# Kernel optimization log

Hardware: AMD Instinct MI355X
Metric: run time of the kernel (lower is better)

The kernel has to match this reference:

```python
import jax, jax.numpy as jnp
import numpy as np

ALPHA = 0.25
GAMMA = 2.0
W_CLASS = 2.0
W_BBOX = 5.0
W_GIOU = 2.0
EPS_LOG = 1e-8
EPS_DIV = 1e-6


def box_cxcywh_to_xyxy(b):
    cx, cy, w, h = b[..., 0], b[..., 1], b[..., 2], b[..., 3]
    return jnp.stack([cx - 0.5 * w, cy - 0.5 * h, cx + 0.5 * w, cy + 0.5 * h], axis=-1)


def generalized_box_iou(b1, b2):
    # b1: [N,4], b2: [M,4], xyxy -> giou [N,M]
    area1 = (b1[:, 2] - b1[:, 0]) * (b1[:, 3] - b1[:, 1])
    area2 = (b2[:, 2] - b2[:, 0]) * (b2[:, 3] - b2[:, 1])
    lt = jnp.maximum(b1[:, None, :2], b2[None, :, :2])
    rb = jnp.minimum(b1[:, None, 2:], b2[None, :, 2:])
    wh = jnp.maximum(rb - lt, 0.0)
    inter = wh[..., 0] * wh[..., 1]
    union = area1[:, None] + area2[None, :] - inter
    iou = inter / jnp.maximum(union, EPS_DIV)
    lt_e = jnp.minimum(b1[:, None, :2], b2[None, :, :2])
    rb_e = jnp.maximum(b1[:, None, 2:], b2[None, :, 2:])
    wh_e = jnp.maximum(rb_e - lt_e, 0.0)
    enclosing = wh_e[..., 0] * wh_e[..., 1]
    return iou - (enclosing - union) / jnp.maximum(enclosing, EPS_DIV)


def setup_inputs() -> dict:
    key = jax.random.key(0)
    k1, k2, k3, k4 = jax.random.split(key, 4)
    B, Q, C, T = 16, 900, 91, 4800  # T = 16 images * 300 targets
    pred_logits = jax.random.normal(k1, (B, Q, C), dtype=jnp.float32)
    pred_boxes = jax.random.uniform(k2, (B, Q, 4), dtype=jnp.float32)  # cxcywh in [0,1]
    tgt_ids = jax.random.randint(k3, (T,), 1, C + 1)  # 1-based labels (code uses tgt_ids - 1)
    tgt_boxes = jax.random.uniform(k4, (T, 4), dtype=jnp.float32)
    return {"pred_logits": pred_logits, "pred_boxes": pred_boxes,
            "tgt_ids": tgt_ids, "tgt_boxes": tgt_boxes}


def reference(pred_logits, pred_boxes, tgt_ids, tgt_boxes):
    B, Q, C = pred_logits.shape
    pl = jax.nn.sigmoid(pred_logits.reshape(B * Q, C))   # [BQ, C]
    pb = pred_boxes.reshape(B * Q, 4)                    # [BQ, 4]

    # focal-style class cost
    neg_cost = (1.0 - ALPHA) * pl ** GAMMA * (-jnp.log(1.0 - pl + EPS_LOG))
    pos_cost = ALPHA * (1.0 - pl) ** GAMMA * (-jnp.log(pl + EPS_LOG))
    cost_class = (pos_cost - neg_cost)[:, tgt_ids - 1]   # [BQ, T]

    # L1 box cost (cdist, p=1)
    cost_bbox = jnp.sum(jnp.abs(pb[:, None, :] - tgt_boxes[None, :, :]), axis=-1)  # [BQ, T]

    # negative generalized IoU cost
    cost_giou = -generalized_box_iou(box_cxcywh_to_xyxy(pb), box_cxcywh_to_xyxy(tgt_boxes))

    Cmat = W_CLASS * cost_class + W_BBOX * cost_bbox + W_GIOU * cost_giou
    return Cmat.reshape(B, Q, -1)  # [B, Q, T]
```

## Files before the change

### kernel.cpp

```cpp
#include <hip/hip_runtime.h>

typedef float f32x4 __attribute__((ext_vector_type(4)));

constexpr int kB = 16, kQ = 900, kC = 91, kT = 4800;
constexpr int kBQ = kB * kQ;
constexpr int kTI = 16;
constexpr int kJT = 4;
constexpr int kBT = 256;
constexpr int kJB = kBT * kJT;
constexpr int kCDS = 20;

__global__ __launch_bounds__(256)
void class_cost_kernel(const float* __restrict__ logits,
                       float* __restrict__ cd, int n) {
    int idx = blockIdx.x * 256 + threadIdx.x;
    if (idx >= n) return;
    float x = logits[idx];
    float p = 1.0f / (1.0f + expf(-x));
    float omp = 1.0f - p;
    float pos = 0.25f * omp * omp * (-logf(p + 1e-8f));
    float neg = 0.75f * p * p * (-logf(omp + 1e-8f));
    cd[idx] = 2.0f * (pos - neg) + 2.0f;
}

__global__ __launch_bounds__(256, 4)
void cost_kernel(const float* __restrict__ pred_boxes,
                 const int*   __restrict__ tgt_ids,
                 const float* __restrict__ tgt_boxes,
                 const float* __restrict__ cd,
                 float*       __restrict__ out) {
    __shared__ float lds_cdT[kC * kCDS];

    const int tid = threadIdx.x;
    const int i0  = blockIdx.y * kTI;
    const int j0  = blockIdx.x * kJB + tid * kJT;

    for (int k = tid; k < kTI * kC; k += kBT) {
        int i = k / kC, c = k - i * kC;
        lds_cdT[c * kCDS + i] = cd[(i0 + i) * kC + c];
    }
    __syncthreads();

    if (j0 + kJT > kT) return;

    int4 ids = *reinterpret_cast<const int4*>(&tgt_ids[j0]);
    const float* rowp[kJT] = {
        &lds_cdT[(ids.x - 1) * kCDS], &lds_cdT[(ids.y - 1) * kCDS],
        &lds_cdT[(ids.z - 1) * kCDS], &lds_cdT[(ids.w - 1) * kCDS] };

    float tcx[kJT], tcy[kJT], tw[kJT], th[kJT];
    float tx0[kJT], ty0[kJT], tx1[kJT], ty1[kJT], ta[kJT];
    #pragma unroll
    for (int q = 0; q < kJT; ++q) {
        float4 tb = reinterpret_cast<const float4*>(tgt_boxes)[j0 + q];
        tcx[q] = tb.x; tcy[q] = tb.y; tw[q] = tb.z; th[q] = tb.w;
        tx0[q] = tb.x - 0.5f * tb.z;  ty0[q] = tb.y - 0.5f * tb.w;
        tx1[q] = tb.x + 0.5f * tb.z;  ty1[q] = tb.y + 0.5f * tb.w;
        ta[q]  = tb.z * tb.w;
    }

    const size_t row0 = (size_t)i0 * kT + j0;

    #pragma unroll
    for (int ig = 0; ig < kTI / 4; ++ig) {
        f32x4 cdv[kJT];
        #pragma unroll
        for (int q = 0; q < kJT; ++q)
            cdv[q] = *reinterpret_cast<const f32x4*>(rowp[q] + ig * 4);

        #pragma unroll
        for (int i2 = 0; i2 < 4; ++i2) {
            const int ii = ig * 4 + i2;
            const float4 pb = reinterpret_cast<const float4*>(pred_boxes)[i0 + ii];
            const float pcx = pb.x, pcy = pb.y, pw = pb.z, ph = pb.w;
            const float px0 = pcx - 0.5f * pw, py0 = pcy - 0.5f * ph;
            const float px1 = pcx + 0.5f * pw, py1 = pcy + 0.5f * ph;
            const float pa  = pw * ph;

            f32x4 res;
            #pragma unroll
            for (int q = 0; q < kJT; ++q) {
                const float cdvq = cdv[q][i2];

                float dx = pcx - tcx[q], dy = pcy - tcy[q];
                float dw = pw  - tw[q],  dh = ph  - th[q];
                float l1 = (fabsf(dx) + fabsf(dy)) + (fabsf(dw) + fabsf(dh));

                float lx = fmaxf(px0, tx0[q]), ly = fmaxf(py0, ty0[q]);
                float rx = fminf(px1, tx1[q]), ry = fminf(py1, ty1[q]);
                float iwr = rx - lx, ihr = ry - ly;
                float inter = fmaxf(iwr, 0.f) * fmaxf(ihr, 0.f);

                float ew  = (pw + tw[q]) - iwr;
                float eh  = (ph + th[q]) - ihr;
                float enc = ew * eh;
                float uni = (pa + ta[q]) - inter;

                float rcpu = __builtin_amdgcn_rcpf(fmaxf(uni, 1e-6f));
                float rcpe = __builtin_amdgcn_rcpf(fmaxf(enc, 1e-6f));

                float c = fmaf(5.0f, l1, cdvq);
                c = fmaf(-2.0f, inter * rcpu, c);
                c = fmaf(-2.0f, uni * rcpe, c);
                res[q] = c;
            }

            *reinterpret_cast<f32x4*>(&out[row0 + (size_t)ii * kT]) = res;
        }
    }
}

extern "C" void kernel_launch(void* const* d_in, const int* in_sizes, int n_in,
                              void* d_out, int out_size, void* d_ws, size_t ws_size,
                              hipStream_t stream) {
    const float* logits  = (const float*)d_in[0];
    const float* pboxes  = (const float*)d_in[1];
    const int*   tids    = (const int*)d_in[2];
    const float* tboxes  = (const float*)d_in[3];
    float* out = (float*)d_out;
    float* cd  = (float*)d_ws;

    const int n_cd = kBQ * kC;
    class_cost_kernel<<<(n_cd + 255) / 256, 256, 0, stream>>>(logits, cd, n_cd);

    dim3 grid((kT + kJB - 1) / kJB, kBQ / kTI);
    cost_kernel<<<grid, 256, 0, stream>>>(pboxes, tids, tboxes, cd, out);
}
```

Baseline: 308.7 us.

## Fuse class-cost computation into the main cost kernel, loop over target tiles

Removes the separate sigmoid/focal class-cost kernel and its workspace round trip: each block now computes the class costs for its 8 query rows directly into LDS from the logits. Each block then loops over all target tiles instead of one tile per block, so the class-cost tile is computed once per row group rather than reloaded by every target-tile block. Row tile shrinks from 16 to 8 to keep the grid large. This drops a kernel launch and the intermediate array traffic, at the cost of less output work per LDS tile and a serial loop over five target tiles per block.

```diff
diff --git a/kernel.cpp b/kernel.cpp
--- a/kernel.cpp
+++ b/kernel.cpp
@@ -4,108 +4,103 @@
 
 constexpr int kB = 16, kQ = 900, kC = 91, kT = 4800;
 constexpr int kBQ = kB * kQ;
-constexpr int kTI = 16;
+constexpr int kTI = 8;
 constexpr int kJT = 4;
 constexpr int kBT = 256;
 constexpr int kJB = kBT * kJT;
-constexpr int kCDS = 20;
-
-__global__ __launch_bounds__(256)
-void class_cost_kernel(const float* __restrict__ logits,
-                       float* __restrict__ cd, int n) {
-    int idx = blockIdx.x * 256 + threadIdx.x;
-    if (idx >= n) return;
-    float x = logits[idx];
-    float p = 1.0f / (1.0f + expf(-x));
-    float omp = 1.0f - p;
-    float pos = 0.25f * omp * omp * (-logf(p + 1e-8f));
-    float neg = 0.75f * p * p * (-logf(omp + 1e-8f));
-    cd[idx] = 2.0f * (pos - neg) + 2.0f;
-}
+constexpr int kNT = (kT + kJB - 1) / kJB;
+constexpr int kCDS = 12;
 
 __global__ __launch_bounds__(256, 4)
-void cost_kernel(const float* __restrict__ pred_boxes,
-                 const int*   __restrict__ tgt_ids,
-                 const float* __restrict__ tgt_boxes,
-                 const float* __restrict__ cd,
-                 float*       __restrict__ out) {
+void fused_cost_kernel(const float* __restrict__ logits,
+                       const float* __restrict__ pred_boxes,
+                       const int*   __restrict__ tgt_ids,
+                       const float* __restrict__ tgt_boxes,
+                       float*       __restrict__ out) {
     __shared__ float lds_cdT[kC * kCDS];
 
     const int tid = threadIdx.x;
-    const int i0  = blockIdx.y * kTI;
-    const int j0  = blockIdx.x * kJB + tid * kJT;
+    const int i0  = blockIdx.x * kTI;
 
     for (int k = tid; k < kTI * kC; k += kBT) {
+        float x = logits[i0 * kC + k];
+        float p = 1.0f / (1.0f + expf(-x));
+        float omp = 1.0f - p;
+        float pos = 0.25f * omp * omp * (-logf(p + 1e-8f));
+        float neg = 0.75f * p * p * (-logf(omp + 1e-8f));
         int i = k / kC, c = k - i * kC;
-        lds_cdT[c * kCDS + i] = cd[(i0 + i) * kC + c];
+        lds_cdT[c * kCDS + i] = 2.0f * (pos - neg) + 2.0f;
     }
     __syncthreads();
 
-    if (j0 + kJT > kT) return;
+    for (int jt = 0; jt < kNT; ++jt) {
+        const int j0 = jt * kJB + tid * kJT;
+        if (j0 >= kT) continue;
 
-    int4 ids = *reinterpret_cast<const int4*>(&tgt_ids[j0]);
-    const float* rowp[kJT] = {
-        &lds_cdT[(ids.x - 1) * kCDS], &lds_cdT[(ids.y - 1) * kCDS],
-        &lds_cdT[(ids.z - 1) * kCDS], &lds_cdT[(ids.w - 1) * kCDS] };
+        int4 ids = *reinterpret_cast<const int4*>(&tgt_ids[j0]);
+        const float* rowp[kJT] = {
+            &lds_cdT[(ids.x - 1) * kCDS], &lds_cdT[(ids.y - 1) * kCDS],
+            &lds_cdT[(ids.z - 1) * kCDS], &lds_cdT[(ids.w - 1) * kCDS] };
 
-    float tcx[kJT], tcy[kJT], tw[kJT], th[kJT];
-    float tx0[kJT], ty0[kJT], tx1[kJT], ty1[kJT], ta[kJT];
-    #pragma unroll
-    for (int q = 0; q < kJT; ++q) {
-        float4 tb = reinterpret_cast<const float4*>(tgt_boxes)[j0 + q];
-        tcx[q] = tb.x; tcy[q] = tb.y; tw[q] = tb.z; th[q] = tb.w;
-        tx0[q] = tb.x - 0.5f * tb.z;  ty0[q] = tb.y - 0.5f * tb.w;
-        tx1[q] = tb.x + 0.5f * tb.z;  ty1[q] = tb.y + 0.5f * tb.w;
-        ta[q]  = tb.z * tb.w;
-    }
-
-    const size_t row0 = (size_t)i0 * kT + j0;
-
-    #pragma unroll
-    for (int ig = 0; ig < kTI / 4; ++ig) {
-        f32x4 cdv[kJT];
+        float tcx[kJT], tcy[kJT], tw[kJT], th[kJT];
+        float tx0[kJT], ty0[kJT], tx1[kJT], ty1[kJT], ta[kJT];
         #pragma unroll
-        for (int q = 0; q < kJT; ++q)
-            cdv[q] = *reinterpret_cast<const f32x4*>(rowp[q] + ig * 4);
+        for (int q = 0; q < kJT; ++q) {
+            float4 tb = reinterpret_cast<const float4*>(tgt_boxes)[j0 + q];
+            tcx[q] = tb.x; tcy[q] = tb.y; tw[q] = tb.z; th[q] = tb.w;
+            tx0[q] = tb.x - 0.5f * tb.z;  ty0[q] = tb.y - 0.5f * tb.w;
+            tx1[q] = tb.x + 0.5f * tb.z;  ty1[q] = tb.y + 0.5f * tb.w;
+            ta[q]  = tb.z * tb.w;
+        }
 
         #pragma unroll
-        for (int i2 = 0; i2 < 4; ++i2) {
-            const int ii = ig * 4 + i2;
-            const float4 pb = reinterpret_cast<const float4*>(pred_boxes)[i0 + ii];
-            const float pcx = pb.x, pcy = pb.y, pw = pb.z, ph = pb.w;
-            const float px0 = pcx - 0.5f * pw, py0 = pcy - 0.5f * ph;
-            const float px1 = pcx + 0.5f * pw, py1 = pcy + 0.5f * ph;
-            const float pa  = pw * ph;
+        for (int ig = 0; ig < kTI / 4; ++ig) {
+            f32x4 cdv[kJT];
+            #pragma unroll
+            for (int q = 0; q < kJT; ++q)
+                cdv[q] = *reinterpret_cast<const f32x4*>(rowp[q] + ig * 4);
 
-            f32x4 res;
             #pragma unroll
-            for (int q = 0; q < kJT; ++q) {
-                const float cdvq = cdv[q][i2];
+            for (int i2 = 0; i2 < 4; ++i2) {
+                const int ii = ig * 4 + i2;
+                const float4 pb =
+                    reinterpret_cast<const float4*>(pred_boxes)[i0 + ii];
+                const float pcx = pb.x, pcy = pb.y, pw = pb.z, ph = pb.w;
+                const float px0 = pcx - 0.5f * pw, py0 = pcy - 0.5f * ph;
+                const float px1 = pcx + 0.5f * pw, py1 = pcy + 0.5f * ph;
+                const float pa  = pw * ph;
 
-                float dx = pcx - tcx[q], dy = pcy - tcy[q];
-                float dw = pw  - tw[q],  dh = ph  - th[q];
-                float l1 = (fabsf(dx) + fabsf(dy)) + (fabsf(dw) + fabsf(dh));
+                f32x4 res;
+                #pragma unroll
+                for (int q = 0; q < kJT; ++q) {
+                    const float cdvq = cdv[q][i2];
 
-                float lx = fmaxf(px0, tx0[q]), ly = fmaxf(py0, ty0[q]);
-                float rx = fminf(px1, tx1[q]), ry = fminf(py1, ty1[q]);
-                float iwr = rx - lx, ihr = ry - ly;
-                float inter = fmaxf(iwr, 0.f) * fmaxf(ihr, 0.f);
+                    float dx = pcx - tcx[q], dy = pcy - tcy[q];
+                    float dw = pw  - tw[q],  dh = ph  - th[q];
+                    float l1 = (fabsf(dx) + fabsf(dy)) + (fabsf(dw) + fabsf(dh));
 
-                float ew  = (pw + tw[q]) - iwr;
-                float eh  = (ph + th[q]) - ihr;
-                float enc = ew * eh;
-                float uni = (pa + ta[q]) - inter;
+                    float lx = fmaxf(px0, tx0[q]), ly = fmaxf(py0, ty0[q]);
+                    float rx = fminf(px1, tx1[q]), ry = fminf(py1, ty1[q]);
+                    float iwr = rx - lx, ihr = ry - ly;
+                    float inter = fmaxf(iwr, 0.f) * fmaxf(ihr, 0.f);
 
-                float rcpu = __builtin_amdgcn_rcpf(fmaxf(uni, 1e-6f));
-                float rcpe = __builtin_amdgcn_rcpf(fmaxf(enc, 1e-6f));
+                    float ew  = (pw + tw[q]) - iwr;
+                    float eh  = (ph + th[q]) - ihr;
+                    float enc = ew * eh;
+                    float uni = (pa + ta[q]) - inter;
 
-                float c = fmaf(5.0f, l1, cdvq);
-                c = fmaf(-2.0f, inter * rcpu, c);
-                c = fmaf(-2.0f, uni * rcpe, c);
-                res[q] = c;
+                    float rcpu = __builtin_amdgcn_rcpf(fmaxf(uni, 1e-6f));
+                    float rcpe = __builtin_amdgcn_rcpf(fmaxf(enc, 1e-6f));
+
+                    float c = fmaf(5.0f, l1, cdvq);
+                    c = fmaf(-2.0f, inter * rcpu, c);
+                    c = fmaf(-2.0f, uni * rcpe, c);
+                    res[q] = c;
+                }
+
+                unsigned idx = (unsigned)(i0 + ii) * (unsigned)kT + (unsigned)j0;
+                *reinterpret_cast<f32x4*>(&out[idx]) = res;
             }
-
-            *reinterpret_cast<f32x4*>(&out[row0 + (size_t)ii * kT]) = res;
         }
     }
 }
@@ -118,11 +113,8 @@
     const int*   tids    = (const int*)d_in[2];
     const float* tboxes  = (const float*)d_in[3];
     float* out = (float*)d_out;
-    float* cd  = (float*)d_ws;
+    (void)d_ws; (void)ws_size;
 
-    const int n_cd = kBQ * kC;
-    class_cost_kernel<<<(n_cd + 255) / 256, 256, 0, stream>>>(logits, cd, n_cd);
-
-    dim3 grid((kT + kJB - 1) / kJB, kBQ / kTI);
-    cost_kernel<<<grid, 256, 0, stream>>>(pboxes, tids, tboxes, cd, out);
+    fused_cost_kernel<<<kBQ / kTI, kBT, 0, stream>>>(logits, pboxes, tids,
+                                                     tboxes, out);
 }
```

New measurement: 308.1 us. Within noise of the previous version (-0.2%).
